# Performance work log

Hardware: AMD Instinct MI355X
Metric: run time of the kernel (lower is better)

The kernel has to match this reference:

```python
import jax, jax.numpy as jnp
import numpy as np
from jax import lax

B, L, H, F, K, NBINS, MAXLEN = 32, 256, 256, 256, 3, 256, 2048
EPS = 1e-5


def _conv1d(x, w, b):
    # x: [B, L, Cin], w: [K, Cin, Cout] (torch Conv1d 'same' padding = (K-1)//2)
    pad = (w.shape[0] - 1) // 2
    y = lax.conv_general_dilated(x, w, (1,), [(pad, pad)],
                                 dimension_numbers=('NWC', 'WIO', 'NWC'))
    return y + b


def _layernorm(x, g, b):
    m = jnp.mean(x, axis=-1, keepdims=True)
    v = jnp.var(x, axis=-1, keepdims=True)
    return (x - m) * lax.rsqrt(v + EPS) * g + b


def _variance_predictor(x, i, w1, b1, g1, be1, w2, b2, g2, be2, wl, bl, mask):
    # conv -> relu -> LN -> conv -> relu -> LN -> linear -> squeeze -> masked_fill
    h = _layernorm(jax.nn.relu(_conv1d(x, w1[i], b1[i])), g1[i], be1[i])
    h = _layernorm(jax.nn.relu(_conv1d(h, w2[i], b2[i])), g2[i], be2[i])
    out = (h @ wl[i] + bl[i])[..., 0]          # [B, L]
    return jnp.where(mask, 0.0, out)


def _length_regulate(x, duration, max_len):
    # Vectorized replacement for the per-token expand/cat loop:
    # cumsum offsets + parallel gather into a padded buffer.
    cum = jnp.cumsum(duration, axis=1)          # [B, L]
    mel_len = cum[:, -1]                        # [B]
    t = jnp.arange(max_len)                     # [T]
    # phoneme index owning frame t: first position where cum > t
    idx = jax.vmap(lambda c: jnp.searchsorted(c, t, side='right'))(cum)  # [B, T]
    idx = jnp.minimum(idx, x.shape[1] - 1)
    out = jnp.take_along_axis(x, idx[:, :, None], axis=1)  # [B, T, H]
    valid = t[None, :] < mel_len[:, None]                   # [B, T]
    out = out * valid[:, :, None].astype(x.dtype)           # zero padding
    return out, mel_len, ~valid


def setup_inputs() -> dict:
    key = jax.random.key(0)
    ks = jax.random.split(key, 20)
    s = 1.0 / np.sqrt(H)
    inp = {
        'x': jax.random.normal(ks[0], (B, L, H), jnp.float32),
        'pitch_target': jax.random.normal(ks[1], (B, L), jnp.float32),
        'energy_target': jax.random.normal(ks[2], (B, L), jnp.float32),
        # stacked params for the 3 predictors: 0=duration, 1=pitch, 2=energy
        'w1': jax.random.normal(ks[3], (3, K, H, F), jnp.float32) * s,
        'b1': jnp.zeros((3, F), jnp.float32),
        'g1': jnp.ones((3, F), jnp.float32),
        'be1': jnp.zeros((3, F), jnp.float32),
        'w2': jax.random.normal(ks[4], (3, K, F, F), jnp.float32) * s,
        'b2': jnp.zeros((3, F), jnp.float32),
        'g2': jnp.ones((3, F), jnp.float32),
        'be2': jnp.zeros((3, F), jnp.float32),
        'wl': jax.random.normal(ks[5], (3, F, 1), jnp.float32) * s,
        'bl': jnp.zeros((3, 1), jnp.float32),
        'pitch_bins': jnp.linspace(-3.0, 3.0, NBINS - 1, dtype=jnp.float32),
        'energy_bins': jnp.linspace(-3.0, 3.0, NBINS - 1, dtype=jnp.float32),
        'pitch_emb': jax.random.normal(ks[6], (NBINS, H), jnp.float32),
        'energy_emb': jax.random.normal(ks[7], (NBINS, H), jnp.float32),
        'src_mask': jnp.zeros((B, L), bool),
        'duration_target': jax.random.randint(ks[8], (B, L), 0, 8),
        'max_len': MAXLEN,
    }
    return inp


def reference(x, pitch_target, energy_target,
              w1, b1, g1, be1, w2, b2, g2, be2, wl, bl,
              pitch_bins, energy_bins, pitch_emb, energy_emb,
              src_mask, duration_target, max_len):
    p = (w1, b1, g1, be1, w2, b2, g2, be2, wl, bl)
    log_duration_prediction = _variance_predictor(x, 0, *p, src_mask)
    # phoneme-level pitch (training path: target given -> bucketize + embed)
    pitch_prediction = _variance_predictor(x, 1, *p, src_mask)
    pitch_idx = jnp.searchsorted(pitch_bins, pitch_target, side='left')
    x = x + pitch_emb[pitch_idx]
    # phoneme-level energy (predictor sees x AFTER pitch embedding added)
    energy_prediction = _variance_predictor(x, 2, *p, src_mask)
    energy_idx = jnp.searchsorted(energy_bins, energy_target, side='left')
    x = x + energy_emb[energy_idx]
    # length regulator: duration_rounded = duration_target in training
    out, mel_len, mel_mask = _length_regulate(x, duration_target, max_len)
    return out, log_duration_prediction, pitch_prediction, energy_prediction, mel_len, mel_mask
```

## Files before the change

kernel.cpp:

```cpp
#include <hip/hip_runtime.h>
#include <hip/hip_bf16.h>
#include <cstdint>

typedef float f32x4 __attribute__((ext_vector_type(4)));
typedef short bf16x8 __attribute__((ext_vector_type(8)));

#define P_TOT 8192
#define KH 768
#define PADL 258
#define EPS_ 1e-5f

__device__ __forceinline__ unsigned short f2bf(float f) {
    unsigned int x = __float_as_uint(f);
    unsigned int r = (x + 0x7fffu + ((x >> 16) & 1u)) >> 16;
    return (unsigned short)r;
}

__global__ __launch_bounds__(256) void k_pre(
        const float* __restrict__ x, const float* __restrict__ pt, const float* __restrict__ et,
        const float* __restrict__ pbins, const float* __restrict__ ebins,
        const float* __restrict__ pemb, const float* __restrict__ eemb,
        const float* __restrict__ w1, const float* __restrict__ w2,
        const int* __restrict__ dur,
        unsigned short* __restrict__ xplain, unsigned short* __restrict__ xpplain,
        unsigned short* __restrict__ bt,
        float* __restrict__ out, float* __restrict__ maskout, float* __restrict__ mel_len_out) {
    __shared__ char smem[16640];
    const int bx = blockIdx.x;
    const int t = threadIdx.x;

    if (bx < 2048) {
        float* pb = (float*)smem;
        float* eb = pb + 256;
        int*   sc = (int*)(eb + 256);
        const int b = bx >> 6;
        if (t < 255) { pb[t] = pbins[t]; eb[t] = ebins[t]; }
        sc[t] = dur[b * 256 + t];
        for (int s = 1; s < 256; s <<= 1) {
            __syncthreads();
            int add = (t >= s) ? sc[t - s] : 0;
            __syncthreads();
            sc[t] += add;
        }
        __syncthreads();

        int w = t >> 6, lane = t & 63;
        int p = bx * 4 + w; int l = p & 255;
        float ptv = pt[p], etv = et[p];
        int lo = 0, hi = 255;
        while (lo < hi) { int mid = (lo + hi) >> 1; if (pb[mid] < ptv) lo = mid + 1; else hi = mid; }
        int pidx = lo;
        lo = 0; hi = 255;
        while (lo < hi) { int mid = (lo + hi) >> 1; if (eb[mid] < etv) lo = mid + 1; else hi = mid; }
        int eidx = lo;
        f32x4 xv = *(const f32x4*)(x    + (size_t)p * 256 + lane * 4);
        f32x4 pe = *(const f32x4*)(pemb + (size_t)pidx * 256 + lane * 4);
        f32x4 ee = *(const f32x4*)(eemb + (size_t)eidx * 256 + lane * 4);
        f32x4 xpv = xv + pe;
        f32x4 xpev = xpv + ee;
        size_t row = (size_t)b * PADL + 1 + l;
        ushort4 xb, xpb;
        xb.x = f2bf(xv[0]);  xb.y = f2bf(xv[1]);  xb.z = f2bf(xv[2]);  xb.w = f2bf(xv[3]);
        xpb.x = f2bf(xpv[0]); xpb.y = f2bf(xpv[1]); xpb.z = f2bf(xpv[2]); xpb.w = f2bf(xpv[3]);
        *(ushort4*)(xplain  + row * 256 + lane * 4) = xb;
        *(ushort4*)(xpplain + row * 256 + lane * 4) = xpb;
        ushort4 z; z.x = z.y = z.z = z.w = 0;
        if (l == 0) {
            *(ushort4*)(xplain  + ((size_t)b * PADL) * 256 + lane * 4) = z;
            *(ushort4*)(xpplain + ((size_t)b * PADL) * 256 + lane * 4) = z;
        }
        if (l == 255) {
            *(ushort4*)(xplain  + ((size_t)b * PADL + 257) * 256 + lane * 4) = z;
            *(ushort4*)(xpplain + ((size_t)b * PADL + 257) * 256 + lane * 4) = z;
        }
        int start = l ? sc[l - 1] : 0;
        int end = sc[l];
        for (int tt = start; tt < end; ++tt)
            __builtin_nontemporal_store(xpev,
                (f32x4*)(out + ((size_t)(b * 2048 + tt)) * 256 + lane * 4));
    } else if (bx < 2336) {
        float (*tile)[65] = (float(*)[65])smem;
        int id = bx - 2048;
        int tf = id & 3; int th = (id >> 2) & 3;
        int rest = id >> 4;
        int k = rest % 3; rest /= 3;
        int set = rest % 3; int tensor = rest / 3;
        const float* src = tensor ? w2 : w1;
        const float* s = src + (((size_t)set * 3 + k) * 256 + th * 64) * 256 + tf * 64;
        int fl = t & 63;
        int q = t >> 6;
#pragma unroll
        for (int i = 0; i < 16; ++i) {
            int hl = i * 4 + q;
            tile[hl][fl] = s[(size_t)hl * 256 + fl];
        }
        __syncthreads();
        size_t rowbase = (size_t)tensor * 768 + set * 256 + tf * 64;
        size_t colbase = (size_t)k * 256 + th * 64;
#pragma unroll
        for (int i = 0; i < 16; ++i) {
            int f2 = i * 4 + q;
            bt[(rowbase + f2) * KH + colbase + fl] = f2bf(tile[fl][f2]);
        }
    } else if (bx < 2368) {
        int* sh = (int*)smem;
        int b = bx - 2336;
        sh[t] = dur[b * 256 + t];
        __syncthreads();
        for (int s = 128; s > 0; s >>= 1) {
            if (t < s) sh[t] += sh[t + s];
            __syncthreads();
        }
        if (t == 0) mel_len_out[b] = (float)sh[0];
    } else {
        int* sh = (int*)smem;
        int g = bx - 2368;
        int b = g >> 6;
        int t0 = (g & 63) * 32;
        sh[t] = dur[b * 256 + t];
        __syncthreads();
        for (int s = 128; s > 0; s >>= 1) {
            if (t < s) sh[t] += sh[t + s];
            __syncthreads();
        }
        int mel = sh[0];
        int w = t >> 6, lane = t & 63;
        f32x4 z4 = (f32x4){0.f, 0.f, 0.f, 0.f};
#pragma unroll
        for (int it = 0; it < 8; ++it) {
            int tt = t0 + it * 4 + w;
            if (tt >= mel)
                __builtin_nontemporal_store(z4,
                    (f32x4*)(out + ((size_t)(b * 2048 + tt)) * 256 + lane * 4));
        }
        if (t < 32) maskout[b * 2048 + t0 + t] = (t0 + t < mel) ? 0.f : 1.f;
    }
}

__device__ __forceinline__ void stageA128(const unsigned short* __restrict__ A, int browPad,
                                          unsigned short* As, int tid) {
    for (int g = tid; g < 4160; g += 512) {
        int p = g * 16;
        int r = p >> 9;
        int c = (p & 511) ^ ((r & 7) << 4);
        __builtin_amdgcn_global_load_lds(
            (const __attribute__((address_space(1))) unsigned int*)((const char*)(A + (size_t)(browPad + r) * 256) + c),
            (__attribute__((address_space(3))) unsigned int*)((char*)As + p), 16, 0, 0);
    }
}

__device__ __forceinline__ void stageB128(const unsigned short* __restrict__ Bm, int kt,
                                          unsigned short* Bs, int tid) {
#pragma unroll
    for (int j = 0; j < 2; ++j) {
        int p = j * 8192 + tid * 16;
        int c = p >> 6;
        int kb = (p & 63) ^ ((c & 3) << 4);
        __builtin_amdgcn_global_load_lds(
            (const __attribute__((address_space(1))) unsigned int*)((const char*)(Bm + (size_t)c * KH + kt) + kb),
            (__attribute__((address_space(3))) unsigned int*)((char*)Bs + p), 16, 0, 0);
    }
}

__device__ __forceinline__ void compute128(const unsigned short* As, const unsigned short* Bs,
                                           int kt, int lane, int wr, int wc, f32x4 acc[4][4]) {
    const int rsel = lane & 15;
    const int lhi = lane >> 4;
    const int tap = kt >> 8;
    const int hcb = (kt & 255) * 2 + lhi * 16;
    bf16x8 af[4], bfr[4];
#pragma unroll
    for (int m = 0; m < 4; ++m) {
        int r = tap + wr * 64 + m * 16 + rsel;
        af[m] = *(const bf16x8*)((const char*)As + r * 512 + (hcb ^ ((r & 7) << 4)));
    }
#pragma unroll
    for (int n = 0; n < 4; ++n) {
        int c = wc * 64 + n * 16 + rsel;
        bfr[n] = *(const bf16x8*)((const char*)Bs + c * 64 + ((lhi * 16) ^ ((c & 3) << 4)));
    }
#pragma unroll
    for (int m = 0; m < 4; ++m)
#pragma unroll
        for (int n = 0; n < 4; ++n)
            acc[m][n] = __builtin_amdgcn_mfma_f32_16x16x32_bf16(af[m], bfr[n], acc[m][n], 0, 0, 0);
}

__device__ __forceinline__ void conv_kloop(const unsigned short* __restrict__ A,
                                           const unsigned short* __restrict__ Bm,
                                           int browPad, int lane, int wr, int wc, int tid,
                                           unsigned short* As, unsigned short (*Bs)[8192],
                                           f32x4 acc[4][4]) {
    stageB128(Bm, 0, Bs[0], tid);
    stageA128(A, browPad, As, tid);
    stageB128(Bm, 32, Bs[1], tid);
    stageB128(Bm, 64, Bs[2], tid);
#pragma unroll
    for (int t = 0; t < 24; ++t) {
        if (t <= 21)      asm volatile("s_waitcnt vmcnt(4)" ::: "memory");
        else if (t == 22) asm volatile("s_waitcnt vmcnt(2)" ::: "memory");
        else              asm volatile("s_waitcnt vmcnt(0)" ::: "memory");
        __builtin_amdgcn_s_barrier();
        __builtin_amdgcn_sched_barrier(0);
        if (t + 3 < 24)
            stageB128(Bm, (t + 3) * 32, Bs[(t + 3) & 3], tid);
        compute128(As, Bs[t & 3], t * 32, lane, wr, wc, acc);
    }
    __syncthreads();
}

__global__ __launch_bounds__(512) void k_conv_ln1(
        const unsigned short* __restrict__ xplain, const unsigned short* __restrict__ xpplain,
        const unsigned short* __restrict__ bt,
        const float* __restrict__ b1, const float* __restrict__ g1, const float* __restrict__ be1,
        unsigned short* __restrict__ h0, unsigned short* __restrict__ h1, unsigned short* __restrict__ h2) {
    __shared__ unsigned short As[33280];
    __shared__ unsigned short Bs[4][8192];
    __shared__ float2 red[4][128];

    const int pred = blockIdx.y;
    const unsigned short* A  = (pred < 2) ? xplain : xpplain;
    const unsigned short* Bm = bt + (size_t)pred * 256 * KH;
    unsigned short* hout = (pred == 0) ? h0 : (pred == 1) ? h1 : h2;

    const int rowBase = blockIdx.x * 128;
    const int bb = rowBase >> 8;
    const int l0 = rowBase & 255;
    const int browPad = bb * PADL + l0;
    const int tid = threadIdx.x;
    const int lane = tid & 63;
    const int wv = tid >> 6;
    const int wr = wv >> 2, wc = wv & 3;
    const int rsel = lane & 15;
    const int lhi = lane >> 4;

    f32x4 acc[4][4];
#pragma unroll
    for (int m = 0; m < 4; ++m)
#pragma unroll
        for (int n = 0; n < 4; ++n) acc[m][n] = (f32x4){0.f, 0.f, 0.f, 0.f};

    conv_kloop(A, Bm, browPad, lane, wr, wc, tid, As, Bs, acc);

    float bcol[4], gcol[4], becol[4];
#pragma unroll
    for (int n = 0; n < 4; ++n) {
        int c = wc * 64 + n * 16 + rsel;
        bcol[n] = b1[pred * 256 + c];
        gcol[n] = g1[pred * 256 + c];
        becol[n] = be1[pred * 256 + c];
    }

#pragma unroll
    for (int m = 0; m < 4; ++m)
#pragma unroll
        for (int r = 0; r < 4; ++r) {
            float s = 0.f, s2 = 0.f;
#pragma unroll
            for (int n = 0; n < 4; ++n) {
                float v = fmaxf(acc[m][n][r] + bcol[n], 0.f);
                s += v; s2 += v * v;
            }
#pragma unroll
            for (int o = 1; o < 16; o <<= 1) { s += __shfl_xor(s, o); s2 += __shfl_xor(s2, o); }
            if (rsel == 0) red[wc][wr * 64 + m * 16 + lhi * 4 + r] = make_float2(s, s2);
        }
    __syncthreads();
    if (tid < 128) {
        float2 a0 = red[0][tid], a1 = red[1][tid], a2 = red[2][tid], a3 = red[3][tid];
        red[0][tid] = make_float2(a0.x + a1.x + a2.x + a3.x, a0.y + a1.y + a2.y + a3.y);
    }
    __syncthreads();

#pragma unroll
    for (int m = 0; m < 4; ++m)
#pragma unroll
        for (int r = 0; r < 4; ++r) {
            int rl = wr * 64 + m * 16 + lhi * 4 + r;
            float2 t = red[0][rl];
            float mean = t.x * (1.f / 256.f);
            float var = t.y * (1.f / 256.f) - mean * mean;
            float inv = rsqrtf(var + EPS_);
            int l = l0 + rl;
            size_t row = (size_t)bb * PADL + 1 + l;
#pragma unroll
            for (int n = 0; n < 4; ++n) {
                float v = fmaxf(acc[m][n][r] + bcol[n], 0.f);
                float h = (v - mean) * inv * gcol[n] + becol[n];
                int c = wc * 64 + n * 16 + rsel;
                hout[row * 256 + c] = f2bf(h);
                if (l == 0)   hout[((size_t)bb * PADL) * 256 + c] = 0;
                if (l == 255) hout[((size_t)bb * PADL + 257) * 256 + c] = 0;
            }
        }
}

__global__ __launch_bounds__(512) void k_conv_ln2(
        const unsigned short* __restrict__ h0, const unsigned short* __restrict__ h1,
        const unsigned short* __restrict__ h2, const unsigned short* __restrict__ bt,
        const float* __restrict__ b2, const float* __restrict__ g2, const float* __restrict__ be2,
        const float* __restrict__ wl, const float* __restrict__ bl,
        const char* __restrict__ mask, float* __restrict__ outp) {
    __shared__ unsigned short As[33280];
    __shared__ unsigned short Bs[4][8192];
    __shared__ float2 red[4][128];
    __shared__ float  red2[4][128];

    const int pred = blockIdx.y;
    const unsigned short* A  = (pred == 0) ? h0 : (pred == 1) ? h1 : h2;
    const unsigned short* Bm = bt + (size_t)(768 + pred * 256) * KH;

    const int rowBase = blockIdx.x * 128;
    const int bb = rowBase >> 8;
    const int l0 = rowBase & 255;
    const int browPad = bb * PADL + l0;
    const int tid = threadIdx.x;
    const int lane = tid & 63;
    const int wv = tid >> 6;
    const int wr = wv >> 2, wc = wv & 3;
    const int rsel = lane & 15;
    const int lhi = lane >> 4;

    f32x4 acc[4][4];
#pragma unroll
    for (int m = 0; m < 4; ++m)
#pragma unroll
        for (int n = 0; n < 4; ++n) acc[m][n] = (f32x4){0.f, 0.f, 0.f, 0.f};

    conv_kloop(A, Bm, browPad, lane, wr, wc, tid, As, Bs, acc);

    float bcol[4], gcol[4], becol[4], wcol[4];
#pragma unroll
    for (int n = 0; n < 4; ++n) {
        int c = wc * 64 + n * 16 + rsel;
        bcol[n] = b2[pred * 256 + c];
        gcol[n] = g2[pred * 256 + c];
        becol[n] = be2[pred * 256 + c];
        wcol[n] = wl[pred * 256 + c];
    }

#pragma unroll
    for (int m = 0; m < 4; ++m)
#pragma unroll
        for (int r = 0; r < 4; ++r) {
            float s = 0.f, s2 = 0.f;
#pragma unroll
            for (int n = 0; n < 4; ++n) {
                float v = fmaxf(acc[m][n][r] + bcol[n], 0.f);
                s += v; s2 += v * v;
            }
#pragma unroll
            for (int o = 1; o < 16; o <<= 1) { s += __shfl_xor(s, o); s2 += __shfl_xor(s2, o); }
            if (rsel == 0) red[wc][wr * 64 + m * 16 + lhi * 4 + r] = make_float2(s, s2);
        }
    __syncthreads();
    if (tid < 128) {
        float2 a0 = red[0][tid], a1 = red[1][tid], a2 = red[2][tid], a3 = red[3][tid];
        red[0][tid] = make_float2(a0.x + a1.x + a2.x + a3.x, a0.y + a1.y + a2.y + a3.y);
    }
    __syncthreads();

#pragma unroll
    for (int m = 0; m < 4; ++m)
#pragma unroll
        for (int r = 0; r < 4; ++r) {
            int rl = wr * 64 + m * 16 + lhi * 4 + r;
            float2 t = red[0][rl];
            float mean = t.x * (1.f / 256.f);
            float var = t.y * (1.f / 256.f) - mean * mean;
            float inv = rsqrtf(var + EPS_);
            float d = 0.f;
#pragma unroll
            for (int n = 0; n < 4; ++n) {
                float v = fmaxf(acc[m][n][r] + bcol[n], 0.f);
                float h = (v - mean) * inv * gcol[n] + becol[n];
                d += h * wcol[n];
            }
#pragma unroll
            for (int o = 1; o < 16; o <<= 1) d += __shfl_xor(d, o);
            if (rsel == 0) red2[wc][rl] = d;
        }
    __syncthreads();
    if (tid < 128) {
        int p = rowBase + tid;
        float o = red2[0][tid] + red2[1][tid] + red2[2][tid] + red2[3][tid] + bl[pred];
        if (mask[p]) o = 0.f;
        outp[(size_t)pred * P_TOT + p] = o;
    }
}

extern "C" void kernel_launch(void* const* d_in, const int* in_sizes, int n_in,
                              void* d_out, int out_size, void* d_ws, size_t ws_size,
                              hipStream_t stream) {
    const float* x     = (const float*)d_in[0];
    const float* pt    = (const float*)d_in[1];
    const float* et    = (const float*)d_in[2];
    const float* w1    = (const float*)d_in[3];
    const float* b1    = (const float*)d_in[4];
    const float* g1    = (const float*)d_in[5];
    const float* be1   = (const float*)d_in[6];
    const float* w2    = (const float*)d_in[7];
    const float* b2    = (const float*)d_in[8];
    const float* g2    = (const float*)d_in[9];
    const float* be2   = (const float*)d_in[10];
    const float* wl    = (const float*)d_in[11];
    const float* bl    = (const float*)d_in[12];
    const float* pbins = (const float*)d_in[13];
    const float* ebins = (const float*)d_in[14];
    const float* pemb  = (const float*)d_in[15];
    const float* eemb  = (const float*)d_in[16];
    const char*  mask  = (const char*)d_in[17];
    const int*   dur   = (const int*)d_in[18];

    char* ws = (char*)d_ws;
    unsigned short* xplain  = (unsigned short*)(ws + 0);
    unsigned short* xpplain = (unsigned short*)(ws + 8388608);
    unsigned short* h0      = (unsigned short*)(ws + 16777216);
    unsigned short* h1      = (unsigned short*)(ws + 25165824);
    unsigned short* h2      = (unsigned short*)(ws + 33554432);
    unsigned short* btall   = (unsigned short*)(ws + 52428800);

    float* out        = (float*)d_out;
    float* out_pred   = out + 16777216;
    float* out_mellen = out + 16801792;
    float* out_mask   = out + 16801824;

    hipLaunchKernelGGL(k_pre, dim3(4416), dim3(256), 0, stream,
                       x, pt, et, pbins, ebins, pemb, eemb, w1, w2, dur,
                       xplain, xpplain, btall, out, out_mask, out_mellen);

    hipLaunchKernelGGL(k_conv_ln1, dim3(64, 3), dim3(512), 0, stream,
                       xplain, xpplain, btall, b1, g1, be1, h0, h1, h2);

    hipLaunchKernelGGL(k_conv_ln2, dim3(64, 3), dim3(512), 0, stream,
                       h0, h1, h2, btall, b2, g2, be2, wl, bl, mask, out_pred);
}
```

Before: 63.56 us.

## Move padding zero-fill into conv kernels' idle CUs and swizzle block mapping

Moves the zero-fill of padded output frames and the mel mask out of the preprocessing kernel and into 64 extra workgroups in each conv kernel. There the writes run on CUs left idle by the 192-block GEMM grid, split between the two conv launches. The conv grids are flattened to 1D with a swizzle that interleaves predictors across blocks. MFMA sections are raised to higher wave priority with s_setprio. The cost is that the zero-fill stores now compete for memory bandwidth with the GEMM loads.

```diff
diff --git a/kernel.cpp b/kernel.cpp
--- a/kernel.cpp
+++ b/kernel.cpp
@@ -24,7 +24,7 @@
         const int* __restrict__ dur,
         unsigned short* __restrict__ xplain, unsigned short* __restrict__ xpplain,
         unsigned short* __restrict__ bt,
-        float* __restrict__ out, float* __restrict__ maskout, float* __restrict__ mel_len_out) {
+        float* __restrict__ out, float* __restrict__ mel_len_out) {
     __shared__ char smem[16640];
     const int bx = blockIdx.x;
     const int t = threadIdx.x;
@@ -102,7 +102,7 @@
             int f2 = i * 4 + q;
             bt[(rowbase + f2) * KH + colbase + fl] = f2bf(tile[fl][f2]);
         }
-    } else if (bx < 2368) {
+    } else {
         int* sh = (int*)smem;
         int b = bx - 2336;
         sh[t] = dur[b * 256 + t];
@@ -112,28 +112,6 @@
             __syncthreads();
         }
         if (t == 0) mel_len_out[b] = (float)sh[0];
-    } else {
-        int* sh = (int*)smem;
-        int g = bx - 2368;
-        int b = g >> 6;
-        int t0 = (g & 63) * 32;
-        sh[t] = dur[b * 256 + t];
-        __syncthreads();
-        for (int s = 128; s > 0; s >>= 1) {
-            if (t < s) sh[t] += sh[t + s];
-            __syncthreads();
-        }
-        int mel = sh[0];
-        int w = t >> 6, lane = t & 63;
-        f32x4 z4 = (f32x4){0.f, 0.f, 0.f, 0.f};
-#pragma unroll
-        for (int it = 0; it < 8; ++it) {
-            int tt = t0 + it * 4 + w;
-            if (tt >= mel)
-                __builtin_nontemporal_store(z4,
-                    (f32x4*)(out + ((size_t)(b * 2048 + tt)) * 256 + lane * 4));
-        }
-        if (t < 32) maskout[b * 2048 + t0 + t] = (t0 + t < mel) ? 0.f : 1.f;
     }
 }
 
@@ -169,6 +147,7 @@
     const int tap = kt >> 8;
     const int hcb = (kt & 255) * 2 + lhi * 16;
     bf16x8 af[4], bfr[4];
+    __builtin_amdgcn_s_setprio(1);
 #pragma unroll
     for (int m = 0; m < 4; ++m) {
         int r = tap + wr * 64 + m * 16 + rsel;
@@ -184,6 +163,7 @@
 #pragma unroll
         for (int n = 0; n < 4; ++n)
             acc[m][n] = __builtin_amdgcn_mfma_f32_16x16x32_bf16(af[m], bfr[n], acc[m][n], 0, 0, 0);
+    __builtin_amdgcn_s_setprio(0);
 }
 
 __device__ __forceinline__ void conv_kloop(const unsigned short* __restrict__ A,
@@ -209,25 +189,58 @@
     __syncthreads();
 }
 
+__device__ __forceinline__ void zero_role(const int* __restrict__ dur, float* __restrict__ out,
+                                          float* __restrict__ maskout, int b, int t0,
+                                          int* sh, int tid) {
+    if (tid < 256) sh[tid] = dur[b * 256 + tid];
+    __syncthreads();
+    for (int s = 128; s > 0; s >>= 1) {
+        if (tid < s) sh[tid] += sh[tid + s];
+        __syncthreads();
+    }
+    int mel = sh[0];
+    int wv8 = tid >> 6, lane = tid & 63;
+    f32x4 z4 = (f32x4){0.f, 0.f, 0.f, 0.f};
+#pragma unroll 4
+    for (int it = 0; it < 64; ++it) {
+        int tt = t0 + it * 8 + wv8;
+        if (tt >= mel)
+            __builtin_nontemporal_store(z4,
+                (f32x4*)(out + ((size_t)(b * 2048 + tt)) * 256 + lane * 4));
+    }
+    maskout[b * 2048 + t0 + tid] = (t0 + tid < mel) ? 0.f : 1.f;
+}
+
 __global__ __launch_bounds__(512) void k_conv_ln1(
         const unsigned short* __restrict__ xplain, const unsigned short* __restrict__ xpplain,
         const unsigned short* __restrict__ bt,
         const float* __restrict__ b1, const float* __restrict__ g1, const float* __restrict__ be1,
-        unsigned short* __restrict__ h0, unsigned short* __restrict__ h1, unsigned short* __restrict__ h2) {
+        unsigned short* __restrict__ h0, unsigned short* __restrict__ h1, unsigned short* __restrict__ h2,
+        const int* __restrict__ dur, float* __restrict__ out, float* __restrict__ maskout) {
     __shared__ unsigned short As[33280];
     __shared__ unsigned short Bs[4][8192];
     __shared__ float2 red[4][128];
 
-    const int pred = blockIdx.y;
+    const int wg = blockIdx.x;
+    const int tid = threadIdx.x;
+
+    if (wg >= 192) {
+        int z = wg - 192;
+        zero_role(dur, out, maskout, (z >> 2), (z & 3) * 512, (int*)As, tid);
+        return;
+    }
+    const int swz = (wg & 7) * 24 + (wg >> 3);
+    const int pred = swz >> 6;
+    const int px = swz & 63;
+
     const unsigned short* A  = (pred < 2) ? xplain : xpplain;
     const unsigned short* Bm = bt + (size_t)pred * 256 * KH;
     unsigned short* hout = (pred == 0) ? h0 : (pred == 1) ? h1 : h2;
 
-    const int rowBase = blockIdx.x * 128;
+    const int rowBase = px * 128;
     const int bb = rowBase >> 8;
     const int l0 = rowBase & 255;
     const int browPad = bb * PADL + l0;
-    const int tid = threadIdx.x;
     const int lane = tid & 63;
     const int wv = tid >> 6;
     const int wr = wv >> 2, wc = wv & 3;
@@ -300,21 +313,32 @@
         const unsigned short* __restrict__ h2, const unsigned short* __restrict__ bt,
         const float* __restrict__ b2, const float* __restrict__ g2, const float* __restrict__ be2,
         const float* __restrict__ wl, const float* __restrict__ bl,
-        const char* __restrict__ mask, float* __restrict__ outp) {
+        const char* __restrict__ mask, float* __restrict__ outp,
+        const int* __restrict__ dur, float* __restrict__ out, float* __restrict__ maskout) {
     __shared__ unsigned short As[33280];
     __shared__ unsigned short Bs[4][8192];
     __shared__ float2 red[4][128];
     __shared__ float  red2[4][128];
 
-    const int pred = blockIdx.y;
+    const int wg = blockIdx.x;
+    const int tid = threadIdx.x;
+
+    if (wg >= 192) {
+        int z = wg - 192;
+        zero_role(dur, out, maskout, 16 + (z >> 2), (z & 3) * 512, (int*)As, tid);
+        return;
+    }
+    const int swz = (wg & 7) * 24 + (wg >> 3);
+    const int pred = swz >> 6;
+    const int px = swz & 63;
+
     const unsigned short* A  = (pred == 0) ? h0 : (pred == 1) ? h1 : h2;
     const unsigned short* Bm = bt + (size_t)(768 + pred * 256) * KH;
 
-    const int rowBase = blockIdx.x * 128;
+    const int rowBase = px * 128;
     const int bb = rowBase >> 8;
     const int l0 = rowBase & 255;
     const int browPad = bb * PADL + l0;
-    const int tid = threadIdx.x;
     const int lane = tid & 63;
     const int wv = tid >> 6;
     const int wr = wv >> 2, wc = wv & 3;
@@ -425,13 +449,15 @@
     float* out_mellen = out + 16801792;
     float* out_mask   = out + 16801824;
 
-    hipLaunchKernelGGL(k_pre, dim3(4416), dim3(256), 0, stream,
+    hipLaunchKernelGGL(k_pre, dim3(2368), dim3(256), 0, stream,
                        x, pt, et, pbins, ebins, pemb, eemb, w1, w2, dur,
-                       xplain, xpplain, btall, out, out_mask, out_mellen);
-
-    hipLaunchKernelGGL(k_conv_ln1, dim3(64, 3), dim3(512), 0, stream,
-                       xplain, xpplain, btall, b1, g1, be1, h0, h1, h2);
-
-    hipLaunchKernelGGL(k_conv_ln2, dim3(64, 3), dim3(512), 0, stream,
-                       h0, h1, h2, btall, b2, g2, be2, wl, bl, mask, out_pred);
-}
+                       xplain, xpplain, btall, out, out_mellen);
+
+    hipLaunchKernelGGL(k_conv_ln1, dim3(256), dim3(512), 0, stream,
+                       xplain, xpplain, btall, b1, g1, be1, h0, h1, h2,
+                       dur, out, out_mask);
+
+    hipLaunchKernelGGL(k_conv_ln2, dim3(256), dim3(512), 0, stream,
+                       h0, h1, h2, btall, b2, g2, be2, wl, bl, mask, out_pred,
+                       dur, out, out_mask);
+}
```

Result: no change. 64.25 us (+1.1%).
